# Kernel optimization log

Measured on AMD Instinct MI355X. Metric: run time of the kernel, lower is better.

The kernel has to match this reference:

```python
import jax, jax.numpy as jnp
import numpy as np

D_MODEL = 1024
N_HEAD = 16
D_K = D_MODEL // N_HEAD
B, S = 2, 2048
NEG = -1000000000.0


def setup_inputs() -> dict:
    key = jax.random.key(0)
    ks = jax.random.split(key, 9)
    inp = {
        "input_q": jax.random.normal(ks[0], (B, S, D_MODEL), dtype=jnp.float32),
        "input_k": jax.random.normal(ks[1], (B, S, D_MODEL), dtype=jnp.float32),
        "input_v": jax.random.normal(ks[2], (B, S, D_MODEL), dtype=jnp.float32),
        "mask": jax.random.randint(ks[3], (1, 1, S, S), 0, 2, dtype=jnp.int32),
        # parameters (Linear weights stored as [in, out] for x @ W)
        "w_q": jax.random.normal(ks[4], (D_MODEL, D_MODEL), dtype=jnp.float32) / np.sqrt(D_MODEL),
        "w_k": jax.random.normal(ks[5], (D_MODEL, D_MODEL), dtype=jnp.float32) / np.sqrt(D_MODEL),
        "w_v": jax.random.normal(ks[6], (D_MODEL, D_MODEL), dtype=jnp.float32) / np.sqrt(D_MODEL),
        "w_o": jax.random.normal(ks[7], (D_MODEL, D_MODEL), dtype=jnp.float32) / np.sqrt(D_MODEL),
        "b_o": jax.random.normal(ks[8], (D_MODEL,), dtype=jnp.float32) * 0.01,
    }
    return inp


def reference(input_q, input_k, input_v, mask, w_q, w_k, w_v, w_o, b_o):
    b = input_q.shape[0]
    # QKV projections -> [B, H, S, d_k]
    def split_heads(x):
        return x.reshape(b, -1, N_HEAD, D_K).transpose(0, 2, 1, 3)
    q = split_heads(input_q @ w_q)
    k = split_heads(input_k @ w_k)
    v = split_heads(input_v @ w_v)
    # naive attention: materialize [B, H, Sq, Sk] scores
    scores = jnp.einsum("bhqd,bhkd->bhqk", q, k) / jnp.sqrt(jnp.float32(D_K))
    scores = jnp.where(mask == 0, jnp.float32(NEG), scores)
    attn = jax.nn.softmax(scores, axis=-1)
    per_head = jnp.einsum("bhqk,bhkd->bhqd", attn, v)
    concat = per_head.transpose(0, 2, 1, 3).reshape(b, -1, N_HEAD * D_K)
    return concat @ w_o + b_o
```

## Files before the change

### kernel.cpp

```cpp
#include <hip/hip_runtime.h>
#include <hip/hip_bf16.h>

typedef _Float16 halfx8 __attribute__((ext_vector_type(8)));
typedef float floatx4 __attribute__((ext_vector_type(4)));

constexpr int S = 2048;
constexpr int DM = 1024;
constexpr int NH = 16;
constexpr int DK = 64;
constexpr int BATCH = 2;
constexpr int MROWS = BATCH * S;

__global__ void convert_w4(const float* __restrict__ w0, const float* __restrict__ w1,
                           const float* __restrict__ w2, const float* __restrict__ w3,
                           _Float16* __restrict__ o0, _Float16* __restrict__ o1,
                           _Float16* __restrict__ o2, _Float16* __restrict__ o3) {
  const float* w = (blockIdx.z == 0) ? w0 : (blockIdx.z == 1) ? w1 : (blockIdx.z == 2) ? w2 : w3;
  _Float16* wt = (blockIdx.z == 0) ? o0 : (blockIdx.z == 1) ? o1 : (blockIdx.z == 2) ? o2 : o3;
  __shared__ float tile[32][33];
  int n0 = blockIdx.x * 32, k0 = blockIdx.y * 32;
  int tx = threadIdx.x, ty = threadIdx.y;
#pragma unroll
  for (int i = 0; i < 4; ++i)
    tile[ty + i * 8][tx] = w[(k0 + ty + i * 8) * DM + n0 + tx];
  __syncthreads();
#pragma unroll
  for (int i = 0; i < 4; ++i)
    wt[(n0 + ty + i * 8) * DM + k0 + tx] = (_Float16)tile[tx][ty + i * 8];
}

__global__ void convert_in3(const float* __restrict__ a0, const float* __restrict__ a1,
                            const float* __restrict__ a2, _Float16* __restrict__ o0,
                            _Float16* __restrict__ o1, _Float16* __restrict__ o2) {
  const float* a = (blockIdx.z == 0) ? a0 : (blockIdx.z == 1) ? a1 : a2;
  _Float16* o = (blockIdx.z == 0) ? o0 : (blockIdx.z == 1) ? o1 : o2;
  size_t i = ((size_t)blockIdx.x * 256 + threadIdx.x) * 8;
  float4 va = *(const float4*)(a + i);
  float4 vb = *(const float4*)(a + i + 4);
  union { halfx8 v; _Float16 h[8]; } u;
  u.h[0] = (_Float16)va.x; u.h[1] = (_Float16)va.y;
  u.h[2] = (_Float16)va.z; u.h[3] = (_Float16)va.w;
  u.h[4] = (_Float16)vb.x; u.h[5] = (_Float16)vb.y;
  u.h[6] = (_Float16)vb.z; u.h[7] = (_Float16)vb.w;
  *(halfx8*)(o + i) = u.v;
}

__global__ void pack_mask(const int* __restrict__ mask, unsigned* __restrict__ bits) {
  int t = blockIdx.x * 256 + threadIdx.x;
  unsigned long long bal = __ballot(mask[t] != 0);
  int lane = threadIdx.x & 63;
  if (lane == 0) bits[t >> 5] = (unsigned)bal;
  else if (lane == 32) bits[t >> 5] = (unsigned)(bal >> 32);
}

template <int EPI>
__global__ __launch_bounds__(256) void gemm_bt(const _Float16* __restrict__ A,
                                               const _Float16* __restrict__ Bt,
                                               void* __restrict__ Cp,
                                               const float* __restrict__ bias) {
  constexpr int LDT = 72;
  __shared__ __align__(16) _Float16 Asm[128 * LDT];
  __shared__ __align__(16) _Float16 Bsm[64 * LDT];
  const int tid = threadIdx.x;
  const int w = tid >> 6, l = tid & 63, lo = l & 15, quad = l >> 4;
  const int wm = (w >> 1) * 64, wn = (w & 1) * 32;
  const int bm = blockIdx.y * 128, bn = blockIdx.x * 64;

  const int arow = tid >> 1, acol = (tid & 1) * 32;
  const int brow = tid >> 2, bcol = (tid & 3) * 16;

  floatx4 acc[4][2] = {};

  for (int k0 = 0; k0 < DM; k0 += 64) {
#pragma unroll
    for (int i = 0; i < 4; ++i)
      *(halfx8*)&Asm[arow * LDT + acol + i * 8] =
          *(const halfx8*)(A + (size_t)(bm + arow) * DM + k0 + acol + i * 8);
#pragma unroll
    for (int i = 0; i < 2; ++i)
      *(halfx8*)&Bsm[brow * LDT + bcol + i * 8] =
          *(const halfx8*)(Bt + (size_t)(bn + brow) * DM + k0 + bcol + i * 8);
    __syncthreads();

#pragma unroll
    for (int ks = 0; ks < 2; ++ks) {
      halfx8 af[4], bfr[2];
#pragma unroll
      for (int mt = 0; mt < 4; ++mt)
        af[mt] = *(const halfx8*)&Asm[(wm + mt * 16 + lo) * LDT + ks * 32 + quad * 8];
#pragma unroll
      for (int nt = 0; nt < 2; ++nt)
        bfr[nt] = *(const halfx8*)&Bsm[(wn + nt * 16 + lo) * LDT + ks * 32 + quad * 8];
#pragma unroll
      for (int mt = 0; mt < 4; ++mt)
#pragma unroll
        for (int nt = 0; nt < 2; ++nt)
          acc[mt][nt] =
              __builtin_amdgcn_mfma_f32_16x16x32_f16(af[mt], bfr[nt], acc[mt][nt], 0, 0, 0);
    }
    __syncthreads();
  }

  if constexpr (EPI == 2) {
    constexpr int LDTT = 136;
    _Float16* tb = Asm;
#pragma unroll
    for (int mt = 0; mt < 4; ++mt)
#pragma unroll
      for (int nt = 0; nt < 2; ++nt)
#pragma unroll
        for (int r = 0; r < 4; ++r) {
          int c = wn + nt * 16 + lo;
          int m = wm + mt * 16 + quad * 4 + r;
          tb[c * LDTT + m] = (_Float16)acc[mt][nt][r];
        }
    __syncthreads();
    const int b = bm >> 11, s0 = bm & (S - 1), h = bn >> 6;
    const int d = tid >> 2, chunk = (tid & 3) * 32;
    _Float16* O = (_Float16*)Cp + ((size_t)(b * NH + h) * DK + d) * S + s0 + chunk;
#pragma unroll
    for (int j = 0; j < 4; ++j)
      *(halfx8*)(O + j * 8) = *(const halfx8*)&tb[d * LDTT + chunk + j * 8];
    return;
  }

#pragma unroll
  for (int mt = 0; mt < 4; ++mt)
#pragma unroll
    for (int nt = 0; nt < 2; ++nt)
#pragma unroll
      for (int r = 0; r < 4; ++r) {
        int row = bm + wm + mt * 16 + quad * 4 + r;
        int col = bn + wn + nt * 16 + lo;
        float v = acc[mt][nt][r];
        if constexpr (EPI == 3) {
          ((float*)Cp)[(size_t)row * DM + col] = v + bias[col];
        } else {
          int b = row >> 11, s = row & (S - 1);
          int h = col >> 6, d = col & (DK - 1);
          _Float16* O = (_Float16*)Cp;
          if constexpr (EPI == 0)
            O[((size_t)(b * NH + h) * S + s) * DK + d] = (_Float16)(v * 0.125f);
          if constexpr (EPI == 1)
            O[((size_t)(b * NH + h) * S + s) * DK + d] = (_Float16)v;
        }
      }
}

__global__ __launch_bounds__(256) void attn_kernel(const _Float16* __restrict__ Q,
                                                   const _Float16* __restrict__ Kh,
                                                   const _Float16* __restrict__ Vt,
                                                   const unsigned* __restrict__ bits,
                                                   _Float16* __restrict__ concat) {
  constexpr int LDT = 72;
  __shared__ __align__(16) _Float16 Ksm[64 * LDT];
  __shared__ __align__(16) _Float16 Vsm[64 * LDT];
  __shared__ __align__(16) _Float16 Psm[4 * 16 * LDT];

  const int tid = threadIdx.x;
  const int w = tid >> 6, l = tid & 63, lo = l & 15, quad = l >> 4;
  const int qb = blockIdx.x * 64 + w * 16;
  const int h = blockIdx.y, b = blockIdx.z;

  const _Float16* Qb = Q + (size_t)(b * NH + h) * S * DK;
  const _Float16* Kb = Kh + (size_t)(b * NH + h) * S * DK;
  const _Float16* Vb = Vt + (size_t)(b * NH + h) * DK * S;

  halfx8 qf[2];
#pragma unroll
  for (int ks = 0; ks < 2; ++ks)
    qf[ks] = *(const halfx8*)(Qb + (qb + lo) * DK + ks * 32 + quad * 8);

  floatx4 Oacc[4] = {};
  float lsum[4] = {0.f, 0.f, 0.f, 0.f};

  const int srow = tid >> 2, scol = (tid & 3) * 16;

  for (int kt = 0; kt < S / 64; ++kt) {
#pragma unroll
    for (int i = 0; i < 2; ++i) {
      *(halfx8*)&Ksm[srow * LDT + scol + i * 8] =
          *(const halfx8*)(Kb + (kt * 64 + srow) * DK + scol + i * 8);
      *(halfx8*)&Vsm[srow * LDT + scol + i * 8] =
          *(const halfx8*)(Vb + srow * S + kt * 64 + scol + i * 8);
    }
    __syncthreads();

    floatx4 Sacc[4] = {};
#pragma unroll
    for (int ks = 0; ks < 2; ++ks)
#pragma unroll
      for (int nt = 0; nt < 4; ++nt) {
        halfx8 kf = *(const halfx8*)&Ksm[(nt * 16 + lo) * LDT + ks * 32 + quad * 8];
        Sacc[nt] = __builtin_amdgcn_mfma_f32_16x16x32_f16(qf[ks], kf, Sacc[nt], 0, 0, 0);
      }

#pragma unroll
    for (int r = 0; r < 4; ++r) {
      int q = qb + quad * 4 + r;
      unsigned w0 = bits[q * (S / 32) + kt * 2];
      unsigned w1 = bits[q * (S / 32) + kt * 2 + 1];
#pragma unroll
      for (int nt = 0; nt < 4; ++nt) {
        unsigned word = (nt < 2) ? w0 : w1;
        int bit = ((nt & 1) << 4) + lo;
        float p = ((word >> bit) & 1u) ? __expf(Sacc[nt][r]) : 0.f;
        lsum[r] += p;
        Psm[w * 16 * LDT + (quad * 4 + r) * LDT + nt * 16 + lo] = (_Float16)p;
      }
    }

#pragma unroll
    for (int ks = 0; ks < 2; ++ks) {
      halfx8 pf = *(const halfx8*)&Psm[w * 16 * LDT + lo * LDT + ks * 32 + quad * 8];
#pragma unroll
      for (int nt = 0; nt < 4; ++nt) {
        halfx8 vf = *(const halfx8*)&Vsm[(nt * 16 + lo) * LDT + ks * 32 + quad * 8];
        Oacc[nt] = __builtin_amdgcn_mfma_f32_16x16x32_f16(pf, vf, Oacc[nt], 0, 0, 0);
      }
    }
    __syncthreads();
  }

#pragma unroll
  for (int r = 0; r < 4; ++r)
#pragma unroll
    for (int off = 1; off < 16; off <<= 1) lsum[r] += __shfl_xor(lsum[r], off);

#pragma unroll
  for (int nt = 0; nt < 4; ++nt)
#pragma unroll
    for (int r = 0; r < 4; ++r) {
      int q = qb + quad * 4 + r;
      int d = nt * 16 + lo;
      concat[((size_t)b * S + q) * DM + h * DK + d] = (_Float16)(Oacc[nt][r] / lsum[r]);
    }
}

extern "C" void kernel_launch(void* const* d_in, const int* in_sizes, int n_in,
                              void* d_out, int out_size, void* d_ws, size_t ws_size,
                              hipStream_t stream) {
  const float* in_q = (const float*)d_in[0];
  const float* in_k = (const float*)d_in[1];
  const float* in_v = (const float*)d_in[2];
  const int* mask = (const int*)d_in[3];
  const float* w_q = (const float*)d_in[4];
  const float* w_k = (const float*)d_in[5];
  const float* w_v = (const float*)d_in[6];
  const float* w_o = (const float*)d_in[7];
  const float* b_o = (const float*)d_in[8];
  float* out = (float*)d_out;

  char* ws = (char*)d_ws;
  constexpr size_t WBYTES = (size_t)DM * DM * sizeof(_Float16);
  constexpr size_t MASKBYTES = (size_t)S * (S / 32) * sizeof(unsigned);
  constexpr size_t TBYTES = (size_t)MROWS * DM * sizeof(_Float16);
  _Float16* wtq = (_Float16*)(ws);
  _Float16* wtk = (_Float16*)(ws + WBYTES);
  _Float16* wtv = (_Float16*)(ws + 2 * WBYTES);
  _Float16* wto = (_Float16*)(ws + 3 * WBYTES);
  unsigned* bits = (unsigned*)(ws + 4 * WBYTES);
  char* p = ws + 4 * WBYTES + MASKBYTES;
  _Float16* Qh = (_Float16*)(p);
  _Float16* Kh = (_Float16*)(p + TBYTES);
  _Float16* Vt = (_Float16*)(p + 2 * TBYTES);
  _Float16* concat = (_Float16*)(p + 3 * TBYTES);
  _Float16* xq = (_Float16*)(p + 4 * TBYTES);
  _Float16* xk = (_Float16*)(p + 5 * TBYTES);
  _Float16* xv = (_Float16*)(p + 6 * TBYTES);

  convert_w4<<<dim3(32, 32, 4), dim3(32, 8), 0, stream>>>(w_q, w_k, w_v, w_o,
                                                          wtq, wtk, wtv, wto);
  convert_in3<<<dim3(MROWS * DM / 8 / 256, 1, 3), 256, 0, stream>>>(in_q, in_k, in_v,
                                                                    xq, xk, xv);
  pack_mask<<<(S * S) / 256, 256, 0, stream>>>(mask, bits);

  dim3 ggrid(DM / 64, MROWS / 128);
  gemm_bt<0><<<ggrid, 256, 0, stream>>>(xq, wtq, Qh, nullptr);
  gemm_bt<1><<<ggrid, 256, 0, stream>>>(xk, wtk, Kh, nullptr);
  gemm_bt<2><<<ggrid, 256, 0, stream>>>(xv, wtv, Vt, nullptr);
  attn_kernel<<<dim3(S / 64, NH, BATCH), 256, 0, stream>>>(Qh, Kh, Vt, bits, concat);
  gemm_bt<3><<<ggrid, 256, 0, stream>>>(concat, wto, out, b_o);
}
```

Measured before the change: 285.6 us.

## Fuse QKV projections into one GEMM and streamline attention softmax with exp2 and fp16 mask

Merges the three projection GEMMs into a single launch with 128x128 tiles over concatenated weights. The Q scale is folded together with log2(e) so attention can use exp2. The bit-packed mask is replaced by an fp16 0/1 mask that multiplies packed half2 probabilities. The S=K·Q operand order is swapped so each lane holds contiguous keys, which allows packed half4 stores to the P buffer and a single fdot2-based row-sum. This removes launches and per-element bit extraction, but the fp16 mask makes the attention loop read more mask bytes, and the concat buffer now reuses xq's memory.

```diff
diff --git a/kernel.cpp b/kernel.cpp
--- a/kernel.cpp
+++ b/kernel.cpp
@@ -2,6 +2,9 @@
 #include <hip/hip_bf16.h>
 
 typedef _Float16 halfx8 __attribute__((ext_vector_type(8)));
+typedef _Float16 halfx4 __attribute__((ext_vector_type(4)));
+typedef _Float16 half2t __attribute__((ext_vector_type(2)));
+typedef __fp16 fp16x2 __attribute__((ext_vector_type(2)));
 typedef float floatx4 __attribute__((ext_vector_type(4)));
 
 constexpr int S = 2048;
@@ -9,7 +12,18 @@
 constexpr int NH = 16;
 constexpr int DK = 64;
 constexpr int BATCH = 2;
-constexpr int MROWS = BATCH * S;
+constexpr int MROWS = 4096;
+constexpr float QSCALE = 0.125f * 1.44269504088896340736f;
+
+#if defined(__has_builtin)
+#if __has_builtin(__builtin_amdgcn_fdot2)
+#define HAVE_FDOT2 1
+#endif
+#endif
+
+static __device__ inline half2t pack2(float a, float b) {
+  return __builtin_bit_cast(half2t, __builtin_amdgcn_cvt_pkrtz(a, b));
+}
 
 __global__ void convert_w4(const float* __restrict__ w0, const float* __restrict__ w1,
                            const float* __restrict__ w2, const float* __restrict__ w3,
@@ -45,19 +59,216 @@
   *(halfx8*)(o + i) = u.v;
 }
 
-__global__ void pack_mask(const int* __restrict__ mask, unsigned* __restrict__ bits) {
-  int t = blockIdx.x * 256 + threadIdx.x;
-  unsigned long long bal = __ballot(mask[t] != 0);
-  int lane = threadIdx.x & 63;
-  if (lane == 0) bits[t >> 5] = (unsigned)bal;
-  else if (lane == 32) bits[t >> 5] = (unsigned)(bal >> 32);
-}
-
-template <int EPI>
-__global__ __launch_bounds__(256) void gemm_bt(const _Float16* __restrict__ A,
-                                               const _Float16* __restrict__ Bt,
-                                               void* __restrict__ Cp,
-                                               const float* __restrict__ bias) {
+__global__ void mask_fp16(const int* __restrict__ m, _Float16* __restrict__ Mh) {
+  size_t i = ((size_t)blockIdx.x * 256 + threadIdx.x) * 8;
+  int4 a = *(const int4*)(m + i);
+  int4 b = *(const int4*)(m + i + 4);
+  union { halfx8 v; _Float16 h[8]; } u;
+  u.h[0] = (_Float16)(a.x != 0); u.h[1] = (_Float16)(a.y != 0);
+  u.h[2] = (_Float16)(a.z != 0); u.h[3] = (_Float16)(a.w != 0);
+  u.h[4] = (_Float16)(b.x != 0); u.h[5] = (_Float16)(b.y != 0);
+  u.h[6] = (_Float16)(b.z != 0); u.h[7] = (_Float16)(b.w != 0);
+  *(halfx8*)(Mh + i) = u.v;
+}
+
+__global__ __launch_bounds__(256) void qkv_gemm(const _Float16* __restrict__ xq,
+                                                const _Float16* __restrict__ xk,
+                                                const _Float16* __restrict__ xv,
+                                                const _Float16* __restrict__ wqkv,
+                                                _Float16* __restrict__ Qh,
+                                                _Float16* __restrict__ Kh,
+                                                _Float16* __restrict__ Vt) {
+  constexpr int LDT = 72;
+  __shared__ __align__(16) _Float16 smem[2 * 128 * LDT];
+  _Float16* Asm = smem;
+  _Float16* Bsm = smem + 128 * LDT;
+  const int tid = threadIdx.x;
+  const int w = tid >> 6, l = tid & 63, lo = l & 15, quad = l >> 4;
+  const int wm = (w >> 1) * 64, wn = (w & 1) * 64;
+  const int bx = blockIdx.x, bm = blockIdx.y * 128;
+  const int wid = bx >> 3;
+  const _Float16* A = (wid == 0) ? xq : (wid == 1) ? xk : xv;
+  const _Float16* Bt = wqkv + (size_t)bx * 128 * DM;
+
+  const int srow = tid >> 1, scol = (tid & 1) * 32;
+  const _Float16* Aptr = A + (size_t)(bm + srow) * DM + scol;
+  const _Float16* Bptr = Bt + (size_t)srow * DM + scol;
+
+  floatx4 acc[4][4] = {};
+
+  for (int k0 = 0; k0 < DM; k0 += 64) {
+#pragma unroll
+    for (int i = 0; i < 4; ++i)
+      *(halfx8*)&Asm[srow * LDT + scol + i * 8] = *(const halfx8*)(Aptr + k0 + i * 8);
+#pragma unroll
+    for (int i = 0; i < 4; ++i)
+      *(halfx8*)&Bsm[srow * LDT + scol + i * 8] = *(const halfx8*)(Bptr + k0 + i * 8);
+    __syncthreads();
+
+#pragma unroll
+    for (int ks = 0; ks < 2; ++ks) {
+      halfx8 af[4], bf[4];
+#pragma unroll
+      for (int mt = 0; mt < 4; ++mt)
+        af[mt] = *(const halfx8*)&Asm[(wm + mt * 16 + lo) * LDT + ks * 32 + quad * 8];
+#pragma unroll
+      for (int nt = 0; nt < 4; ++nt)
+        bf[nt] = *(const halfx8*)&Bsm[(wn + nt * 16 + lo) * LDT + ks * 32 + quad * 8];
+#pragma unroll
+      for (int mt = 0; mt < 4; ++mt)
+#pragma unroll
+        for (int nt = 0; nt < 4; ++nt)
+          acc[mt][nt] =
+              __builtin_amdgcn_mfma_f32_16x16x32_f16(af[mt], bf[nt], acc[mt][nt], 0, 0, 0);
+    }
+    __syncthreads();
+  }
+
+  if (wid == 2) {
+    constexpr int LDTT = 136;
+    _Float16* tb = smem;
+#pragma unroll
+    for (int mt = 0; mt < 4; ++mt)
+#pragma unroll
+      for (int nt = 0; nt < 4; ++nt)
+#pragma unroll
+        for (int r = 0; r < 4; ++r) {
+          int dl = wn + nt * 16 + lo;
+          int sl = wm + mt * 16 + quad * 4 + r;
+          tb[dl * LDTT + sl] = (_Float16)acc[mt][nt][r];
+        }
+    __syncthreads();
+    const int b = bm >> 11, s0 = bm & (S - 1);
+    const int d2 = tid >> 1, chunk = (tid & 1) * 64;
+    const int dg = ((bx & 7) * 128 + d2);
+    const int h = dg >> 6, dd = dg & 63;
+    _Float16* O = Vt + ((size_t)(b * NH + h) * DK + dd) * S + s0 + chunk;
+#pragma unroll
+    for (int j = 0; j < 8; ++j)
+      *(halfx8*)(O + j * 8) = *(const halfx8*)&tb[d2 * LDTT + chunk + j * 8];
+    return;
+  }
+
+  _Float16* Out = (wid == 0) ? Qh : Kh;
+  const float scale = (wid == 0) ? QSCALE : 1.0f;
+#pragma unroll
+  for (int mt = 0; mt < 4; ++mt)
+#pragma unroll
+    for (int nt = 0; nt < 4; ++nt)
+#pragma unroll
+      for (int r = 0; r < 4; ++r) {
+        int row = bm + wm + mt * 16 + quad * 4 + r;
+        int n = (bx & 7) * 128 + wn + nt * 16 + lo;
+        int b = row >> 11, s = row & (S - 1);
+        int h = n >> 6, d = n & 63;
+        Out[((size_t)(b * NH + h) * S + s) * DK + d] = (_Float16)(acc[mt][nt][r] * scale);
+      }
+}
+
+__global__ __launch_bounds__(256) void attn_kernel(const _Float16* __restrict__ Q,
+                                                   const _Float16* __restrict__ Kh,
+                                                   const _Float16* __restrict__ Vt,
+                                                   const _Float16* __restrict__ Mh,
+                                                   _Float16* __restrict__ concat) {
+  constexpr int LDT = 72;
+  __shared__ __align__(16) _Float16 Ksm[64 * LDT];
+  __shared__ __align__(16) _Float16 Vsm[64 * LDT];
+  __shared__ __align__(16) _Float16 Psm[4 * 16 * LDT];
+
+  const int tid = threadIdx.x;
+  const int w = tid >> 6, l = tid & 63, lo = l & 15, quad = l >> 4;
+  const int qb = blockIdx.x * 64 + w * 16;
+  const int h = blockIdx.y, b = blockIdx.z;
+
+  const _Float16* Qb = Q + (size_t)(b * NH + h) * S * DK;
+  const _Float16* Kb = Kh + (size_t)(b * NH + h) * S * DK;
+  const _Float16* Vb = Vt + (size_t)(b * NH + h) * DK * S;
+  const _Float16* Mq = Mh + (size_t)(qb + lo) * S;
+
+  halfx8 qf[2];
+#pragma unroll
+  for (int ks = 0; ks < 2; ++ks)
+    qf[ks] = *(const halfx8*)(Qb + (qb + lo) * DK + ks * 32 + quad * 8);
+
+  floatx4 Oacc[4] = {};
+  float lsum = 0.f;
+  const half2t onev = {(_Float16)1.0f, (_Float16)1.0f};
+
+  const int srow = tid >> 2, scol = (tid & 3) * 16;
+  const _Float16* Kp = Kb + srow * DK + scol;
+  const _Float16* Vp = Vb + srow * S + scol;
+  _Float16* Pw = &Psm[w * 16 * LDT];
+
+  for (int kt = 0; kt < S / 64; ++kt) {
+#pragma unroll
+    for (int i = 0; i < 2; ++i) {
+      *(halfx8*)&Ksm[srow * LDT + scol + i * 8] = *(const halfx8*)(Kp + kt * 64 * DK + i * 8);
+      *(halfx8*)&Vsm[srow * LDT + scol + i * 8] = *(const halfx8*)(Vp + kt * 64 + i * 8);
+    }
+    __syncthreads();
+
+    floatx4 Sacc[4] = {};
+#pragma unroll
+    for (int ks = 0; ks < 2; ++ks)
+#pragma unroll
+      for (int nt = 0; nt < 4; ++nt) {
+        halfx8 kf = *(const halfx8*)&Ksm[(nt * 16 + lo) * LDT + ks * 32 + quad * 8];
+        Sacc[nt] = __builtin_amdgcn_mfma_f32_16x16x32_f16(kf, qf[ks], Sacc[nt], 0, 0, 0);
+      }
+
+#pragma unroll
+    for (int nt = 0; nt < 4; ++nt) {
+      union { halfx4 v; half2t h[2]; } mv;
+      mv.v = *(const halfx4*)(Mq + kt * 64 + nt * 16 + quad * 4);
+      half2t p01 = pack2(__builtin_exp2f(Sacc[nt][0]), __builtin_exp2f(Sacc[nt][1]));
+      half2t p23 = pack2(__builtin_exp2f(Sacc[nt][2]), __builtin_exp2f(Sacc[nt][3]));
+      p01 *= mv.h[0];
+      p23 *= mv.h[1];
+#ifdef HAVE_FDOT2
+      lsum = __builtin_amdgcn_fdot2(__builtin_bit_cast(fp16x2, p01),
+                                    __builtin_bit_cast(fp16x2, onev), lsum, false);
+      lsum = __builtin_amdgcn_fdot2(__builtin_bit_cast(fp16x2, p23),
+                                    __builtin_bit_cast(fp16x2, onev), lsum, false);
+#else
+      lsum += (float)p01[0] + (float)p01[1] + (float)p23[0] + (float)p23[1];
+#endif
+      union { halfx4 v; half2t h[2]; } u;
+      u.h[0] = p01; u.h[1] = p23;
+      *(halfx4*)&Pw[lo * LDT + nt * 16 + quad * 4] = u.v;
+    }
+
+#pragma unroll
+    for (int ks = 0; ks < 2; ++ks) {
+      halfx8 pf = *(const halfx8*)&Pw[lo * LDT + ks * 32 + quad * 8];
+#pragma unroll
+      for (int nt = 0; nt < 4; ++nt) {
+        halfx8 vf = *(const halfx8*)&Vsm[(nt * 16 + lo) * LDT + ks * 32 + quad * 8];
+        Oacc[nt] = __builtin_amdgcn_mfma_f32_16x16x32_f16(pf, vf, Oacc[nt], 0, 0, 0);
+      }
+    }
+    __syncthreads();
+  }
+
+  lsum += __shfl_xor(lsum, 16);
+  lsum += __shfl_xor(lsum, 32);
+
+#pragma unroll
+  for (int r = 0; r < 4; ++r) {
+    float lr = __shfl(lsum, quad * 4 + r);
+    float inv = __builtin_amdgcn_rcpf(lr);
+    int q = qb + quad * 4 + r;
+#pragma unroll
+    for (int nt = 0; nt < 4; ++nt) {
+      int d = nt * 16 + lo;
+      concat[((size_t)b * S + q) * DM + h * DK + d] = (_Float16)(Oacc[nt][r] * inv);
+    }
+  }
+}
+
+__global__ __launch_bounds__(256) void out_gemm(const _Float16* __restrict__ A,
+                                                const _Float16* __restrict__ Bt,
+                                                float* __restrict__ Cp,
+                                                const float* __restrict__ bias) {
   constexpr int LDT = 72;
   __shared__ __align__(16) _Float16 Asm[128 * LDT];
   __shared__ __align__(16) _Float16 Bsm[64 * LDT];
@@ -101,29 +312,6 @@
     __syncthreads();
   }
 
-  if constexpr (EPI == 2) {
-    constexpr int LDTT = 136;
-    _Float16* tb = Asm;
-#pragma unroll
-    for (int mt = 0; mt < 4; ++mt)
-#pragma unroll
-      for (int nt = 0; nt < 2; ++nt)
-#pragma unroll
-        for (int r = 0; r < 4; ++r) {
-          int c = wn + nt * 16 + lo;
-          int m = wm + mt * 16 + quad * 4 + r;
-          tb[c * LDTT + m] = (_Float16)acc[mt][nt][r];
-        }
-    __syncthreads();
-    const int b = bm >> 11, s0 = bm & (S - 1), h = bn >> 6;
-    const int d = tid >> 2, chunk = (tid & 3) * 32;
-    _Float16* O = (_Float16*)Cp + ((size_t)(b * NH + h) * DK + d) * S + s0 + chunk;
-#pragma unroll
-    for (int j = 0; j < 4; ++j)
-      *(halfx8*)(O + j * 8) = *(const halfx8*)&tb[d * LDTT + chunk + j * 8];
-    return;
-  }
-
 #pragma unroll
   for (int mt = 0; mt < 4; ++mt)
 #pragma unroll
@@ -132,109 +320,8 @@
       for (int r = 0; r < 4; ++r) {
         int row = bm + wm + mt * 16 + quad * 4 + r;
         int col = bn + wn + nt * 16 + lo;
-        float v = acc[mt][nt][r];
-        if constexpr (EPI == 3) {
-          ((float*)Cp)[(size_t)row * DM + col] = v + bias[col];
-        } else {
-          int b = row >> 11, s = row & (S - 1);
-          int h = col >> 6, d = col & (DK - 1);
-          _Float16* O = (_Float16*)Cp;
-          if constexpr (EPI == 0)
-            O[((size_t)(b * NH + h) * S + s) * DK + d] = (_Float16)(v * 0.125f);
-          if constexpr (EPI == 1)
-            O[((size_t)(b * NH + h) * S + s) * DK + d] = (_Float16)v;
-        }
+        Cp[(size_t)row * DM + col] = acc[mt][nt][r] + bias[col];
       }
-}
-
-__global__ __launch_bounds__(256) void attn_kernel(const _Float16* __restrict__ Q,
-                                                   const _Float16* __restrict__ Kh,
-                                                   const _Float16* __restrict__ Vt,
-                                                   const unsigned* __restrict__ bits,
-                                                   _Float16* __restrict__ concat) {
-  constexpr int LDT = 72;
-  __shared__ __align__(16) _Float16 Ksm[64 * LDT];
-  __shared__ __align__(16) _Float16 Vsm[64 * LDT];
-  __shared__ __align__(16) _Float16 Psm[4 * 16 * LDT];
-
-  const int tid = threadIdx.x;
-  const int w = tid >> 6, l = tid & 63, lo = l & 15, quad = l >> 4;
-  const int qb = blockIdx.x * 64 + w * 16;
-  const int h = blockIdx.y, b = blockIdx.z;
-
-  const _Float16* Qb = Q + (size_t)(b * NH + h) * S * DK;
-  const _Float16* Kb = Kh + (size_t)(b * NH + h) * S * DK;
-  const _Float16* Vb = Vt + (size_t)(b * NH + h) * DK * S;
-
-  halfx8 qf[2];
-#pragma unroll
-  for (int ks = 0; ks < 2; ++ks)
-    qf[ks] = *(const halfx8*)(Qb + (qb + lo) * DK + ks * 32 + quad * 8);
-
-  floatx4 Oacc[4] = {};
-  float lsum[4] = {0.f, 0.f, 0.f, 0.f};
-
-  const int srow = tid >> 2, scol = (tid & 3) * 16;
-
-  for (int kt = 0; kt < S / 64; ++kt) {
-#pragma unroll
-    for (int i = 0; i < 2; ++i) {
-      *(halfx8*)&Ksm[srow * LDT + scol + i * 8] =
-          *(const halfx8*)(Kb + (kt * 64 + srow) * DK + scol + i * 8);
-      *(halfx8*)&Vsm[srow * LDT + scol + i * 8] =
-          *(const halfx8*)(Vb + srow * S + kt * 64 + scol + i * 8);
-    }
-    __syncthreads();
-
-    floatx4 Sacc[4] = {};
-#pragma unroll
-    for (int ks = 0; ks < 2; ++ks)
-#pragma unroll
-      for (int nt = 0; nt < 4; ++nt) {
-        halfx8 kf = *(const halfx8*)&Ksm[(nt * 16 + lo) * LDT + ks * 32 + quad * 8];
-        Sacc[nt] = __builtin_amdgcn_mfma_f32_16x16x32_f16(qf[ks], kf, Sacc[nt], 0, 0, 0);
-      }
-
-#pragma unroll
-    for (int r = 0; r < 4; ++r) {
-      int q = qb + quad * 4 + r;
-      unsigned w0 = bits[q * (S / 32) + kt * 2];
-      unsigned w1 = bits[q * (S / 32) + kt * 2 + 1];
-#pragma unroll
-      for (int nt = 0; nt < 4; ++nt) {
-        unsigned word = (nt < 2) ? w0 : w1;
-        int bit = ((nt & 1) << 4) + lo;
-        float p = ((word >> bit) & 1u) ? __expf(Sacc[nt][r]) : 0.f;
-        lsum[r] += p;
-        Psm[w * 16 * LDT + (quad * 4 + r) * LDT + nt * 16 + lo] = (_Float16)p;
-      }
-    }
-
-#pragma unroll
-    for (int ks = 0; ks < 2; ++ks) {
-      halfx8 pf = *(const halfx8*)&Psm[w * 16 * LDT + lo * LDT + ks * 32 + quad * 8];
-#pragma unroll
-      for (int nt = 0; nt < 4; ++nt) {
-        halfx8 vf = *(const halfx8*)&Vsm[(nt * 16 + lo) * LDT + ks * 32 + quad * 8];
-        Oacc[nt] = __builtin_amdgcn_mfma_f32_16x16x32_f16(pf, vf, Oacc[nt], 0, 0, 0);
-      }
-    }
-    __syncthreads();
-  }
-
-#pragma unroll
-  for (int r = 0; r < 4; ++r)
-#pragma unroll
-    for (int off = 1; off < 16; off <<= 1) lsum[r] += __shfl_xor(lsum[r], off);
-
-#pragma unroll
-  for (int nt = 0; nt < 4; ++nt)
-#pragma unroll
-    for (int r = 0; r < 4; ++r) {
-      int q = qb + quad * 4 + r;
-      int d = nt * 16 + lo;
-      concat[((size_t)b * S + q) * DM + h * DK + d] = (_Float16)(Oacc[nt][r] / lsum[r]);
-    }
 }
 
 extern "C" void kernel_launch(void* const* d_in, const int* in_sizes, int n_in,
@@ -252,33 +339,28 @@
   float* out = (float*)d_out;
 
   char* ws = (char*)d_ws;
-  constexpr size_t WBYTES = (size_t)DM * DM * sizeof(_Float16);
-  constexpr size_t MASKBYTES = (size_t)S * (S / 32) * sizeof(unsigned);
-  constexpr size_t TBYTES = (size_t)MROWS * DM * sizeof(_Float16);
-  _Float16* wtq = (_Float16*)(ws);
-  _Float16* wtk = (_Float16*)(ws + WBYTES);
-  _Float16* wtv = (_Float16*)(ws + 2 * WBYTES);
-  _Float16* wto = (_Float16*)(ws + 3 * WBYTES);
-  unsigned* bits = (unsigned*)(ws + 4 * WBYTES);
-  char* p = ws + 4 * WBYTES + MASKBYTES;
+  constexpr size_t WB = (size_t)DM * DM * sizeof(_Float16);
+  constexpr size_t MB_ = (size_t)S * S * sizeof(_Float16);
+  constexpr size_t TB = (size_t)MROWS * DM * sizeof(_Float16);
+  _Float16* wqkv = (_Float16*)(ws);
+  _Float16* wto = (_Float16*)(ws + 3 * WB);
+  _Float16* Mh = (_Float16*)(ws + 4 * WB);
+  char* p = ws + 4 * WB + MB_;
   _Float16* Qh = (_Float16*)(p);
-  _Float16* Kh = (_Float16*)(p + TBYTES);
-  _Float16* Vt = (_Float16*)(p + 2 * TBYTES);
-  _Float16* concat = (_Float16*)(p + 3 * TBYTES);
-  _Float16* xq = (_Float16*)(p + 4 * TBYTES);
-  _Float16* xk = (_Float16*)(p + 5 * TBYTES);
-  _Float16* xv = (_Float16*)(p + 6 * TBYTES);
-
-  convert_w4<<<dim3(32, 32, 4), dim3(32, 8), 0, stream>>>(w_q, w_k, w_v, w_o,
-                                                          wtq, wtk, wtv, wto);
+  _Float16* Kh = (_Float16*)(p + TB);
+  _Float16* Vt = (_Float16*)(p + 2 * TB);
+  _Float16* xq = (_Float16*)(p + 3 * TB);
+  _Float16* xk = (_Float16*)(p + 4 * TB);
+  _Float16* xv = (_Float16*)(p + 5 * TB);
+  _Float16* concat = xq;
+
+  convert_w4<<<dim3(32, 32, 4), dim3(32, 8), 0, stream>>>(
+      w_q, w_k, w_v, w_o, wqkv, wqkv + DM * DM, wqkv + 2 * DM * DM, wto);
   convert_in3<<<dim3(MROWS * DM / 8 / 256, 1, 3), 256, 0, stream>>>(in_q, in_k, in_v,
                                                                     xq, xk, xv);
-  pack_mask<<<(S * S) / 256, 256, 0, stream>>>(mask, bits);
-
-  dim3 ggrid(DM / 64, MROWS / 128);
-  gemm_bt<0><<<ggrid, 256, 0, stream>>>(xq, wtq, Qh, nullptr);
-  gemm_bt<1><<<ggrid, 256, 0, stream>>>(xk, wtk, Kh, nullptr);
-  gemm_bt<2><<<ggrid, 256, 0, stream>>>(xv, wtv, Vt, nullptr);
-  attn_kernel<<<dim3(S / 64, NH, BATCH), 256, 0, stream>>>(Qh, Kh, Vt, bits, concat);
-  gemm_bt<3><<<ggrid, 256, 0, stream>>>(concat, wto, out, b_o);
-}
+  mask_fp16<<<dim3(S * S / 8 / 256), 256, 0, stream>>>(mask, Mh);
+
+  qkv_gemm<<<dim3(24, 32), 256, 0, stream>>>(xq, xk, xv, wqkv, Qh, Kh, Vt);
+  attn_kernel<<<dim3(S / 64, NH, BATCH), 256, 0, stream>>>(Qh, Kh, Vt, Mh, concat);
+  out_gemm<<<dim3(DM / 64, MROWS / 128), 256, 0, stream>>>(concat, wto, out, b_o);
+}
```

Result: slower. 293.7 us (+2.8%).
